# Kernel optimization log

Hardware: AMD Instinct MI355X
Metric: run time of the kernel (lower is better)

## Reference

```python
import jax, jax.numpy as jnp
import numpy as np

B, H, A, S, D, HID = 2048, 64, 32, 32, 200, 200


def setup_inputs() -> dict:
    key = jax.random.key(0)
    ks = jax.random.split(key, 10)
    sc = 0.05  # small init so sigmoid/tanh/exp stay in a sane range
    rn = lambda k, shape: jax.random.normal(k, shape, jnp.float32)
    return {
        'h0': jnp.zeros((B, D), jnp.float32),
        'z0': jnp.zeros((B, S), jnp.float32),
        'actions': rn(ks[0], (B, H, A)),
        'eps': rn(ks[1], (B, H, S)),
        # GRUCell params (PyTorch layout: [3*D, in] / [3*D, D], gate order r,z,n)
        'W_ih': rn(ks[2], (3 * D, S + A)) * sc,
        'b_ih': jnp.zeros((3 * D,), jnp.float32),
        'W_hh': rn(ks[3], (3 * D, D)) * sc,
        'b_hh': jnp.zeros((3 * D,), jnp.float32),
        # prior_net: Linear(D,HID)+ELU, Linear(HID,HID)+ELU
        'W1': rn(ks[4], (HID, D)) * sc, 'b1': jnp.zeros((HID,), jnp.float32),
        'W2': rn(ks[5], (HID, HID)) * sc, 'b2': jnp.zeros((HID,), jnp.float32),
        # prior_mean / prior_logstd heads
        'Wm': rn(ks[6], (S, HID)) * sc, 'bm': jnp.zeros((S,), jnp.float32),
        'Ws': rn(ks[7], (S, HID)) * sc, 'bs': jnp.zeros((S,), jnp.float32),
    }


def reference(h0, z0, actions, eps, W_ih, b_ih, W_hh, b_hh,
              W1, b1, W2, b2, Wm, bm, Ws, bs):
    """imagine_rollout: sequential GRUCell + prior MLP + reparameterized sample.
    Returns [B, H, D+3S] = concat(h, z, prior_mean, prior_std) along last dim."""

    def step(carry, inp):
        h, z = carry
        a, e = inp  # [B,A], [B,S]
        x = jnp.concatenate([z, a], axis=-1)          # [B, S+A]
        gi = x @ W_ih.T + b_ih                        # [B, 3D]
        gh = h @ W_hh.T + b_hh                        # [B, 3D]
        i_r, i_z, i_n = jnp.split(gi, 3, axis=-1)
        h_r, h_z, h_n = jnp.split(gh, 3, axis=-1)
        r = jax.nn.sigmoid(i_r + h_r)
        u = jax.nn.sigmoid(i_z + h_z)
        n = jnp.tanh(i_n + r * h_n)
        h_new = (1.0 - u) * n + u * h                 # [B, D]
        f = jax.nn.elu(h_new @ W1.T + b1)
        f = jax.nn.elu(f @ W2.T + b2)                 # [B, HID]
        mean = f @ Wm.T + bm                          # [B, S]
        logstd = jnp.clip(f @ Ws.T + bs, -10.0, 2.0)
        std = jnp.exp(logstd)
        z_new = mean + std * e                        # reparameterize
        return (h_new, z_new), (h_new, z_new, mean, std)

    a_t = jnp.swapaxes(actions, 0, 1)  # [H, B, A]
    e_t = jnp.swapaxes(eps, 0, 1)      # [H, B, S]
    _, (hs, zs, ms, ss) = jax.lax.scan(step, (h0, z0), (a_t, e_t))
    traj = jnp.concatenate([hs, zs, ms, ss], axis=-1)  # [H, B, D+3S]
    return jnp.swapaxes(traj, 0, 1)                    # [B, H, D+3S]
```

## Files before the change

kernel.cpp:

```cpp
#include <hip/hip_runtime.h>
#include <math.h>

#define B_TOT    2048
#define H_STEPS  64
#define OUT_FEAT 296
#define BT       16
#define NTHR     512

#define OFF_GRU 0
#define OFF_W1  89856
#define OFF_W2  113152
#define OFF_MS  136448
#define WS_DW   143616

typedef _Float16 f16;
typedef _Float16 f16x8 __attribute__((ext_vector_type(8)));
typedef float    f32x4 __attribute__((ext_vector_type(4)));

union U4H8 { uint4 u; f16x8 h; };

__device__ __forceinline__ unsigned pack_h2(float a, float b) {
    union { _Float16 h[2]; unsigned u; } v;
    v.h[0] = (_Float16)a; v.h[1] = (_Float16)b;
    return v.u;
}
__device__ __forceinline__ float sigmoid_f(float x) {
    return __builtin_amdgcn_rcpf(1.0f + __expf(-x));
}
__device__ __forceinline__ float tanh_f(float x) {
    return 1.0f - 2.0f * __builtin_amdgcn_rcpf(1.0f + __expf(2.0f * x));
}

__device__ __forceinline__ float gru_val(const float* Wih, const float* Whh,
                                         int f, int c, int kl) {
    if (f >= 200) return 0.f;
    if (c < 18) {
        int row = (c < 9) ? f : (200 + f);
        int ks  = (c < 9) ? c : (c - 9);
        int k = ks * 32 + kl;
        if (k < 64)  return Wih[row * 64 + k];
        if (k < 264) return Whh[row * 200 + (k - 64)];
        return 0.f;
    } else if (c < 20) {
        int k = (c - 18) * 32 + kl;
        return Wih[(400 + f) * 64 + k];
    } else {
        int k = (c - 18) * 32 + kl;
        if (k < 264) return Whh[(400 + f) * 200 + (k - 64)];
        return 0.f;
    }
}
__device__ __forceinline__ float mlp_val(const float* W, int f, int ks, int kl) {
    int k = ks * 32 + kl;
    return (f < 200 && k < 200) ? W[f * 200 + k] : 0.f;
}
__device__ __forceinline__ float ms_val(const float* Wm, const float* Ws,
                                        int n, int ks, int kl) {
    int k = ks * 32 + kl;
    if (k >= 200) return 0.f;
    return (n < 32) ? Wm[n * 200 + k] : Ws[(n - 32) * 200 + k];
}

__global__ void pack_weights(const float* __restrict__ Wih, const float* __restrict__ Whh,
                             const float* __restrict__ W1, const float* __restrict__ W2,
                             const float* __restrict__ Wm, const float* __restrict__ Ws,
                             unsigned* __restrict__ ws)
{
    int i = blockIdx.x * 256 + threadIdx.x;
    if (i >= WS_DW) return;
    float v0 = 0.f, v1 = 0.f;
    if (i < OFF_W1) {
        int e    = i * 2;
        int tile = e >> 9;
        int r    = e & 511;
        int lane = r >> 3;
        int jx   = r & 7;
        int j = tile / 27, c = tile % 27;
        int n16 = lane & 15, kg = lane >> 4;
        int f = j * 16 + n16;
        v0 = gru_val(Wih, Whh, f, c, kg * 8 + jx);
        v1 = gru_val(Wih, Whh, f, c, kg * 8 + jx + 1);
    } else if (i < OFF_W2) {
        int e = (i - OFF_W1) * 2;
        int tile = e >> 9, r = e & 511, lane = r >> 3, jx = r & 7;
        int j = tile / 7, ks = tile % 7;
        int n16 = lane & 15, kg = lane >> 4;
        int f = j * 16 + n16;
        v0 = mlp_val(W1, f, ks, kg * 8 + jx);
        v1 = mlp_val(W1, f, ks, kg * 8 + jx + 1);
    } else if (i < OFF_MS) {
        int e = (i - OFF_W2) * 2;
        int tile = e >> 9, r = e & 511, lane = r >> 3, jx = r & 7;
        int j = tile / 7, ks = tile % 7;
        int n16 = lane & 15, kg = lane >> 4;
        int f = j * 16 + n16;
        v0 = mlp_val(W2, f, ks, kg * 8 + jx);
        v1 = mlp_val(W2, f, ks, kg * 8 + jx + 1);
    } else {
        int e = (i - OFF_MS) * 2;
        int tile = e >> 9, r = e & 511, lane = r >> 3, jx = r & 7;
        int nt = tile / 7, ks = tile % 7;
        int n16 = lane & 15, kg = lane >> 4;
        int n = nt * 16 + n16;
        v0 = ms_val(Wm, Ws, n, ks, kg * 8 + jx);
        v1 = ms_val(Wm, Ws, n, ks, kg * 8 + jx + 1);
    }
    ws[i] = pack_h2(v0, v1);
}

#define MFMA(a, b, c) __builtin_amdgcn_mfma_f32_16x16x32_f16((a), (b), (c), 0, 0, 0)

__global__ __launch_bounds__(NTHR, 1) void rssm_rollout(
    const float* __restrict__ h0, const float* __restrict__ z0,
    const float* __restrict__ actions, const float* __restrict__ eps,
    const float* __restrict__ b_ih, const float* __restrict__ b_hh,
    const float* __restrict__ b1, const float* __restrict__ b2,
    const float* __restrict__ bm, const float* __restrict__ bs,
    const unsigned* __restrict__ wsu, float* __restrict__ out)
{
    __shared__ __align__(16) f16  Xs[16][296];
    __shared__ __align__(16) f16  F1s[16][232];
    __shared__ __align__(16) f16  F2s[16][232];
    __shared__ float HF[16][210];
    __shared__ float MSB[16][66];
    __shared__ float brzL[208], buzL[208], binL[208], bhnL[208], b1L[208], b2L[208], bmsL[64];

    const int t    = threadIdx.x;
    const int w    = t >> 6;
    const int lane = t & 63;
    const int n16  = lane & 15;
    const int kg   = lane >> 4;
    const int b0   = blockIdx.x * BT;

    const uint4* GW  = (const uint4*)(wsu + OFF_GRU);
    const uint4* W1W = (const uint4*)(wsu + OFF_W1);
    const uint4* W2W = (const uint4*)(wsu + OFF_W2);
    const uint4* MSW = (const uint4*)(wsu + OFF_MS);

    {
        unsigned* p;
        p = (unsigned*)&Xs[0][0];  for (int i = t; i < 16 * 296 / 2; i += NTHR) p[i] = 0u;
        p = (unsigned*)&F1s[0][0]; for (int i = t; i < 16 * 232 / 2; i += NTHR) p[i] = 0u;
        p = (unsigned*)&F2s[0][0]; for (int i = t; i < 16 * 232 / 2; i += NTHR) p[i] = 0u;
        float* q = (float*)&HF[0][0];
        for (int i = t; i < 16 * 210; i += NTHR) q[i] = 0.f;
    }
    if (t < 208) {
        int f = t; bool real = (f < 200);
        brzL[f] = real ? (b_ih[f] + b_hh[f]) : 0.f;
        buzL[f] = real ? (b_ih[200 + f] + b_hh[200 + f]) : 0.f;
        binL[f] = real ? b_ih[400 + f] : 0.f;
        bhnL[f] = real ? b_hh[400 + f] : 0.f;
        b1L[f]  = real ? b1[f] : 0.f;
        b2L[f]  = real ? b2[f] : 0.f;
    }
    if (t < 64) bmsL[t] = (t < 32) ? bm[t] : bs[t - 32];
    __syncthreads();

    if (t < 256) {
        int m = t >> 4, fb = t & 15;
        Xs[m][fb]      = (f16)z0[(b0 + m) * 32 + fb];
        Xs[m][16 + fb] = (f16)z0[(b0 + m) * 32 + 16 + fb];
        Xs[m][32 + fb] = (f16)actions[((b0 + m) * H_STEPS + 0) * 32 + fb];
        Xs[m][48 + fb] = (f16)actions[((b0 + m) * H_STEPS + 0) * 32 + 16 + fb];
        #pragma unroll
        for (int i = 0; i < 13; ++i) {
            int f = fb + 16 * i;
            if (f < 200) {
                float v = h0[(b0 + m) * 200 + f];
                Xs[m][64 + f] = (f16)v;
                HF[m][f] = v;
            }
        }
    }
    __syncthreads();

    for (int step = 0; step < H_STEPS; ++step) {
        const int sp = (step + 1 < H_STEPS) ? step + 1 : step;

        f16x8 A9[9];
        #pragma unroll
        for (int ks = 0; ks < 9; ++ks)
            A9[ks] = *(const f16x8*)&Xs[n16][ks * 32 + kg * 8];

        float ep0 = 0.f, ep1 = 0.f, ac0 = 0.f, ac1 = 0.f;
        if (t < 256) {
            int m_t = t >> 4, fb_t = t & 15;
            ep0 = eps[((b0 + m_t) * H_STEPS + step) * 32 + fb_t];
            ep1 = eps[((b0 + m_t) * H_STEPS + step) * 32 + 16 + fb_t];
            ac0 = actions[((b0 + m_t) * H_STEPS + sp) * 32 + fb_t];
            ac1 = actions[((b0 + m_t) * H_STEPS + sp) * 32 + 16 + fb_t];
        }
        __syncthreads();

        for (int j = w; j < 13; j += 8) {
            const uint4* tb = GW + (size_t)(j * 27) * 64 + lane;
            U4H8 bfr[27];
            #pragma unroll
            for (int c = 0; c < 27; ++c) bfr[c].u = tb[c * 64];
            f32x4 aR = {0.f,0.f,0.f,0.f}, aU = {0.f,0.f,0.f,0.f};
            f32x4 aI = {0.f,0.f,0.f,0.f}, aH = {0.f,0.f,0.f,0.f};
            #pragma unroll
            for (int ks = 0; ks < 9; ++ks) aR = MFMA(A9[ks], bfr[ks].h, aR);
            #pragma unroll
            for (int ks = 0; ks < 9; ++ks) aU = MFMA(A9[ks], bfr[9 + ks].h, aU);
            #pragma unroll
            for (int ks = 0; ks < 2; ++ks) aI = MFMA(A9[ks], bfr[18 + ks].h, aI);
            #pragma unroll
            for (int ks = 0; ks < 7; ++ks) aH = MFMA(A9[2 + ks], bfr[20 + ks].h, aH);
            const int f = 16 * j + n16;
            const float vbrz = brzL[f], vbuz = buzL[f], vbin = binL[f], vbhn = bhnL[f];
            #pragma unroll
            for (int q = 0; q < 4; ++q) {
                int m = kg * 4 + q;
                float r = sigmoid_f(aR[q] + vbrz);
                float u = sigmoid_f(aU[q] + vbuz);
                float n = tanh_f(aI[q] + vbin + r * (aH[q] + vbhn));
                float ho = HF[m][f];
                float hnew = (1.0f - u) * n + u * ho;
                HF[m][f] = hnew;
                Xs[m][64 + f] = (f16)hnew;
                if (f < 200)
                    out[((size_t)(b0 + m) * H_STEPS + step) * OUT_FEAT + f] = hnew;
            }
        }
        __syncthreads();

        {
            f16x8 A7[7];
            #pragma unroll
            for (int ks = 0; ks < 7; ++ks)
                A7[ks] = *(const f16x8*)&Xs[n16][64 + ks * 32 + kg * 8];
            for (int j = w; j < 13; j += 8) {
                const uint4* tb = W1W + (size_t)(j * 7) * 64 + lane;
                U4H8 bfr[7];
                #pragma unroll
                for (int c = 0; c < 7; ++c) bfr[c].u = tb[c * 64];
                f32x4 acc = {0.f,0.f,0.f,0.f};
                #pragma unroll
                for (int ks = 0; ks < 7; ++ks) acc = MFMA(A7[ks], bfr[ks].h, acc);
                const int f = 16 * j + n16;
                const float bb = b1L[f];
                #pragma unroll
                for (int q = 0; q < 4; ++q) {
                    float v = acc[q] + bb;
                    v = (v > 0.f) ? v : (__expf(v) - 1.0f);
                    F1s[kg * 4 + q][f] = (f16)v;
                }
            }
        }
        __syncthreads();

        {
            f16x8 A7[7];
            #pragma unroll
            for (int ks = 0; ks < 7; ++ks)
                A7[ks] = *(const f16x8*)&F1s[n16][ks * 32 + kg * 8];
            for (int j = w; j < 13; j += 8) {
                const uint4* tb = W2W + (size_t)(j * 7) * 64 + lane;
                U4H8 bfr[7];
                #pragma unroll
                for (int c = 0; c < 7; ++c) bfr[c].u = tb[c * 64];
                f32x4 acc = {0.f,0.f,0.f,0.f};
                #pragma unroll
                for (int ks = 0; ks < 7; ++ks) acc = MFMA(A7[ks], bfr[ks].h, acc);
                const int f = 16 * j + n16;
                const float bb = b2L[f];
                #pragma unroll
                for (int q = 0; q < 4; ++q) {
                    float v = acc[q] + bb;
                    v = (v > 0.f) ? v : (__expf(v) - 1.0f);
                    F2s[kg * 4 + q][f] = (f16)v;
                }
            }
        }
        __syncthreads();

        if (w < 4) {
            f16x8 A7[7];
            #pragma unroll
            for (int ks = 0; ks < 7; ++ks)
                A7[ks] = *(const f16x8*)&F2s[n16][ks * 32 + kg * 8];
            const uint4* tb = MSW + (size_t)(w * 7) * 64 + lane;
            U4H8 bfr[7];
            #pragma unroll
            for (int c = 0; c < 7; ++c) bfr[c].u = tb[c * 64];
            f32x4 acc = {0.f,0.f,0.f,0.f};
            #pragma unroll
            for (int ks = 0; ks < 7; ++ks) acc = MFMA(A7[ks], bfr[ks].h, acc);
            const int n = 16 * w + n16;
            const float bb = bmsL[n];
            #pragma unroll
            for (int q = 0; q < 4; ++q) {
                int m = kg * 4 + q;
                float v = acc[q] + bb;
                size_t ob = ((size_t)(b0 + m) * H_STEPS + step) * OUT_FEAT;
                if (n < 32) {
                    MSB[m][n] = v;
                    out[ob + 232 + n] = v;
                } else {
                    float ls = fminf(fmaxf(v, -10.0f), 2.0f);
                    float sd = __expf(ls);
                    MSB[m][n] = sd;
                    out[ob + 264 + (n - 32)] = sd;
                }
            }
        }
        __syncthreads();

        if (t < 256) {
            int m = t >> 4, fb = t & 15;
            float z0v = MSB[m][fb]      + MSB[m][32 + fb] * ep0;
            float z1v = MSB[m][16 + fb] + MSB[m][48 + fb] * ep1;
            size_t ob = ((size_t)(b0 + m) * H_STEPS + step) * OUT_FEAT;
            out[ob + 200 + fb] = z0v;
            out[ob + 216 + fb] = z1v;
            Xs[m][fb]      = (f16)z0v;
            Xs[m][16 + fb] = (f16)z1v;
            Xs[m][32 + fb] = (f16)ac0;
            Xs[m][48 + fb] = (f16)ac1;
        }
        __syncthreads();
    }
}

extern "C" void kernel_launch(void* const* d_in, const int* in_sizes, int n_in,
                              void* d_out, int out_size, void* d_ws, size_t ws_size,
                              hipStream_t stream) {
    const float* h0      = (const float*)d_in[0];
    const float* z0      = (const float*)d_in[1];
    const float* actions = (const float*)d_in[2];
    const float* eps     = (const float*)d_in[3];
    const float* W_ih    = (const float*)d_in[4];
    const float* b_ih    = (const float*)d_in[5];
    const float* W_hh    = (const float*)d_in[6];
    const float* b_hh    = (const float*)d_in[7];
    const float* W1      = (const float*)d_in[8];
    const float* b1      = (const float*)d_in[9];
    const float* W2      = (const float*)d_in[10];
    const float* b2      = (const float*)d_in[11];
    const float* Wm      = (const float*)d_in[12];
    const float* bm      = (const float*)d_in[13];
    const float* Ws      = (const float*)d_in[14];
    const float* bs      = (const float*)d_in[15];

    unsigned* ws = (unsigned*)d_ws;
    float* out = (float*)d_out;

    hipLaunchKernelGGL(pack_weights, dim3(WS_DW / 256), dim3(256), 0, stream,
                       W_ih, W_hh, W1, W2, Wm, Ws, ws);

    hipLaunchKernelGGL(rssm_rollout, dim3(B_TOT / BT), dim3(NTHR), 0, stream,
                       h0, z0, actions, eps, b_ih, b_hh, b1, b2, bm, bs, ws, out);
}
```

Measured before the change: 631.7 us.

## Keep GRU weight tile in registers and prefetch next-stage weights before barriers

```diff
diff --git a/kernel.cpp b/kernel.cpp
--- a/kernel.cpp
+++ b/kernel.cpp
@@ -137,6 +137,15 @@
     const uint4* W2W = (const uint4*)(wsu + OFF_W2);
     const uint4* MSW = (const uint4*)(wsu + OFF_MS);
 
+    U4H8 gq[27];
+    {
+        const uint4* tb = GW + (size_t)(w * 27) * 64 + lane;
+        #pragma unroll
+        for (int c = 0; c < 27; ++c) gq[c].u = tb[c * 64];
+    }
+    const bool hasB = (w < 5);
+    const uint4* tbB = GW + (size_t)((8 + w) * 27) * 64 + lane;
+
     {
         unsigned* p;
         p = (unsigned*)&Xs[0][0];  for (int i = t; i < 16 * 296 / 2; i += NTHR) p[i] = 0u;
@@ -175,6 +184,35 @@
     }
     __syncthreads();
 
+    auto gru_epi = [&](const f32x4& xR, const f32x4& xU, const f32x4& xI,
+                       const f32x4& xH, int j, int step) {
+        const int f = 16 * j + n16;
+        const float vbrz = brzL[f], vbuz = buzL[f], vbin = binL[f], vbhn = bhnL[f];
+        #pragma unroll
+        for (int q = 0; q < 4; ++q) {
+            int m = kg * 4 + q;
+            float r = sigmoid_f(xR[q] + vbrz);
+            float u = sigmoid_f(xU[q] + vbuz);
+            float n = tanh_f(xI[q] + vbin + r * (xH[q] + vbhn));
+            float ho = HF[m][f];
+            float hnew = (1.0f - u) * n + u * ho;
+            HF[m][f] = hnew;
+            Xs[m][64 + f] = (f16)hnew;
+            if (f < 200)
+                out[((size_t)(b0 + m) * H_STEPS + step) * OUT_FEAT + f] = hnew;
+        }
+    };
+    auto mlp_epi = [&](const f32x4& a, int j, const float* bL, f16 (*dst)[232]) {
+        const int f = 16 * j + n16;
+        const float bb = bL[f];
+        #pragma unroll
+        for (int q = 0; q < 4; ++q) {
+            float v = a[q] + bb;
+            v = (v > 0.f) ? v : (__expf(v) - 1.0f);
+            dst[kg * 4 + q][f] = (f16)v;
+        }
+    };
+
     for (int step = 0; step < H_STEPS; ++step) {
         const int sp = (step + 1 < H_STEPS) ? step + 1 : step;
 
@@ -193,36 +231,47 @@
         }
         __syncthreads();
 
-        for (int j = w; j < 13; j += 8) {
-            const uint4* tb = GW + (size_t)(j * 27) * 64 + lane;
-            U4H8 bfr[27];
-            #pragma unroll
-            for (int c = 0; c < 27; ++c) bfr[c].u = tb[c * 64];
-            f32x4 aR = {0.f,0.f,0.f,0.f}, aU = {0.f,0.f,0.f,0.f};
-            f32x4 aI = {0.f,0.f,0.f,0.f}, aH = {0.f,0.f,0.f,0.f};
-            #pragma unroll
-            for (int ks = 0; ks < 9; ++ks) aR = MFMA(A9[ks], bfr[ks].h, aR);
-            #pragma unroll
-            for (int ks = 0; ks < 9; ++ks) aU = MFMA(A9[ks], bfr[9 + ks].h, aU);
-            #pragma unroll
-            for (int ks = 0; ks < 2; ++ks) aI = MFMA(A9[ks], bfr[18 + ks].h, aI);
-            #pragma unroll
-            for (int ks = 0; ks < 7; ++ks) aH = MFMA(A9[2 + ks], bfr[20 + ks].h, aH);
-            const int f = 16 * j + n16;
-            const float vbrz = brzL[f], vbuz = buzL[f], vbin = binL[f], vbhn = bhnL[f];
-            #pragma unroll
-            for (int q = 0; q < 4; ++q) {
-                int m = kg * 4 + q;
-                float r = sigmoid_f(aR[q] + vbrz);
-                float u = sigmoid_f(aU[q] + vbuz);
-                float n = tanh_f(aI[q] + vbin + r * (aH[q] + vbhn));
-                float ho = HF[m][f];
-                float hnew = (1.0f - u) * n + u * ho;
-                HF[m][f] = hnew;
-                Xs[m][64 + f] = (f16)hnew;
-                if (f < 200)
-                    out[((size_t)(b0 + m) * H_STEPS + step) * OUT_FEAT + f] = hnew;
-            }
+        U4H8 bB1[14], bB2[13];
+        if (hasB) {
+            #pragma unroll
+            for (int c = 0; c < 14; ++c) bB1[c].u = tbB[c * 64];
+        }
+        f32x4 aR = {0.f,0.f,0.f,0.f}, aU = {0.f,0.f,0.f,0.f};
+        f32x4 aI = {0.f,0.f,0.f,0.f}, aH = {0.f,0.f,0.f,0.f};
+        #pragma unroll
+        for (int ks = 0; ks < 9; ++ks) aR = MFMA(A9[ks], gq[ks].h, aR);
+        #pragma unroll
+        for (int ks = 0; ks < 9; ++ks) aU = MFMA(A9[ks], gq[9 + ks].h, aU);
+        #pragma unroll
+        for (int ks = 0; ks < 2; ++ks) aI = MFMA(A9[ks], gq[18 + ks].h, aI);
+        #pragma unroll
+        for (int ks = 0; ks < 7; ++ks) aH = MFMA(A9[2 + ks], gq[20 + ks].h, aH);
+
+        f32x4 aR2 = {0.f,0.f,0.f,0.f}, aU2 = {0.f,0.f,0.f,0.f};
+        f32x4 aI2 = {0.f,0.f,0.f,0.f}, aH2 = {0.f,0.f,0.f,0.f};
+        if (hasB) {
+            #pragma unroll
+            for (int ks = 0; ks < 9; ++ks) aR2 = MFMA(A9[ks], bB1[ks].h, aR2);
+            #pragma unroll
+            for (int ks = 0; ks < 5; ++ks) aU2 = MFMA(A9[ks], bB1[9 + ks].h, aU2);
+            #pragma unroll
+            for (int c = 0; c < 13; ++c) bB2[c].u = tbB[(14 + c) * 64];
+        }
+        gru_epi(aR, aU, aI, aH, w, step);
+        if (hasB) {
+            #pragma unroll
+            for (int ks = 5; ks < 9; ++ks) aU2 = MFMA(A9[ks], bB2[ks - 5].h, aU2);
+            #pragma unroll
+            for (int ks = 0; ks < 2; ++ks) aI2 = MFMA(A9[ks], bB2[4 + ks].h, aI2);
+            #pragma unroll
+            for (int ks = 0; ks < 7; ++ks) aH2 = MFMA(A9[2 + ks], bB2[6 + ks].h, aH2);
+            gru_epi(aR2, aU2, aI2, aH2, 8 + w, step);
+        }
+        U4H8 m1A[7];
+        {
+            const uint4* t1 = W1W + (size_t)(w * 7) * 64 + lane;
+            #pragma unroll
+            for (int c = 0; c < 7; ++c) m1A[c].u = t1[c * 64];
         }
         __syncthreads();
 
@@ -231,23 +280,28 @@
             #pragma unroll
             for (int ks = 0; ks < 7; ++ks)
                 A7[ks] = *(const f16x8*)&Xs[n16][64 + ks * 32 + kg * 8];
-            for (int j = w; j < 13; j += 8) {
-                const uint4* tb = W1W + (size_t)(j * 7) * 64 + lane;
-                U4H8 bfr[7];
+            U4H8 m1B[7];
+            const uint4* t1B = W1W + (size_t)((8 + w) * 7) * 64 + lane;
+            if (hasB) {
                 #pragma unroll
-                for (int c = 0; c < 7; ++c) bfr[c].u = tb[c * 64];
-                f32x4 acc = {0.f,0.f,0.f,0.f};
+                for (int c = 0; c < 7; ++c) m1B[c].u = t1B[c * 64];
+            }
+            f32x4 a1 = {0.f,0.f,0.f,0.f};
+            #pragma unroll
+            for (int ks = 0; ks < 7; ++ks) a1 = MFMA(A7[ks], m1A[ks].h, a1);
+            mlp_epi(a1, w, b1L, F1s);
+            if (hasB) {
+                f32x4 a1B = {0.f,0.f,0.f,0.f};
                 #pragma unroll
-                for (int ks = 0; ks < 7; ++ks) acc = MFMA(A7[ks], bfr[ks].h, acc);
-                const int f = 16 * j + n16;
-                const float bb = b1L[f];
-                #pragma unroll
-                for (int q = 0; q < 4; ++q) {
-                    float v = acc[q] + bb;
-                    v = (v > 0.f) ? v : (__expf(v) - 1.0f);
-                    F1s[kg * 4 + q][f] = (f16)v;
-                }
-            }
+                for (int ks = 0; ks < 7; ++ks) a1B = MFMA(A7[ks], m1B[ks].h, a1B);
+                mlp_epi(a1B, 8 + w, b1L, F1s);
+            }
+        }
+        U4H8 m2A[7];
+        {
+            const uint4* t2 = W2W + (size_t)(w * 7) * 64 + lane;
+            #pragma unroll
+            for (int c = 0; c < 7; ++c) m2A[c].u = t2[c * 64];
         }
         __syncthreads();
 
@@ -256,23 +310,28 @@
             #pragma unroll
             for (int ks = 0; ks < 7; ++ks)
                 A7[ks] = *(const f16x8*)&F1s[n16][ks * 32 + kg * 8];
-            for (int j = w; j < 13; j += 8) {
-                const uint4* tb = W2W + (size_t)(j * 7) * 64 + lane;
-                U4H8 bfr[7];
+            U4H8 m2B[7];
+            const uint4* t2B = W2W + (size_t)((8 + w) * 7) * 64 + lane;
+            if (hasB) {
                 #pragma unroll
-                for (int c = 0; c < 7; ++c) bfr[c].u = tb[c * 64];
-                f32x4 acc = {0.f,0.f,0.f,0.f};
+                for (int c = 0; c < 7; ++c) m2B[c].u = t2B[c * 64];
+            }
+            f32x4 a2 = {0.f,0.f,0.f,0.f};
+            #pragma unroll
+            for (int ks = 0; ks < 7; ++ks) a2 = MFMA(A7[ks], m2A[ks].h, a2);
+            mlp_epi(a2, w, b2L, F2s);
+            if (hasB) {
+                f32x4 a2B = {0.f,0.f,0.f,0.f};
                 #pragma unroll
-                for (int ks = 0; ks < 7; ++ks) acc = MFMA(A7[ks], bfr[ks].h, acc);
-                const int f = 16 * j + n16;
-                const float bb = b2L[f];
-                #pragma unroll
-                for (int q = 0; q < 4; ++q) {
-                    float v = acc[q] + bb;
-                    v = (v > 0.f) ? v : (__expf(v) - 1.0f);
-                    F2s[kg * 4 + q][f] = (f16)v;
-                }
-            }
+                for (int ks = 0; ks < 7; ++ks) a2B = MFMA(A7[ks], m2B[ks].h, a2B);
+                mlp_epi(a2B, 8 + w, b2L, F2s);
+            }
+        }
+        U4H8 msA[7];
+        if (w < 4) {
+            const uint4* tm = MSW + (size_t)(w * 7) * 64 + lane;
+            #pragma unroll
+            for (int c = 0; c < 7; ++c) msA[c].u = tm[c * 64];
         }
         __syncthreads();
 
@@ -281,13 +340,9 @@
             #pragma unroll
             for (int ks = 0; ks < 7; ++ks)
                 A7[ks] = *(const f16x8*)&F2s[n16][ks * 32 + kg * 8];
-            const uint4* tb = MSW + (size_t)(w * 7) * 64 + lane;
-            U4H8 bfr[7];
-            #pragma unroll
-            for (int c = 0; c < 7; ++c) bfr[c].u = tb[c * 64];
             f32x4 acc = {0.f,0.f,0.f,0.f};
             #pragma unroll
-            for (int ks = 0; ks < 7; ++ks) acc = MFMA(A7[ks], bfr[ks].h, acc);
+            for (int ks = 0; ks < 7; ++ks) acc = MFMA(A7[ks], msA[ks].h, acc);
             const int n = 16 * w + n16;
             const float bb = bmsL[n];
             #pragma unroll
```

Result: slower. 2.406 ms (+280.8%).
